# Kernel optimization log

Measured on AMD Instinct MI355X. Metric: run time of the kernel, lower is better.

## Reference

```python
import jax, jax.numpy as jnp
import numpy as np

N_NODES = 50000


def _gcn(x, row, col, w, b, n):
    # add self loops
    loops = jnp.arange(n, dtype=row.dtype)
    row = jnp.concatenate([row, loops])
    col = jnp.concatenate([col, loops])
    h = x @ w  # [N, out]
    deg = jax.ops.segment_sum(jnp.ones(col.shape, h.dtype), col, num_segments=n)
    dinv = jnp.where(deg > 0, deg ** -0.5, 0.0)
    norm = dinv[row] * dinv[col]  # [E+N]
    msg = norm[:, None] * h[row]
    out = jax.ops.segment_sum(msg, col, num_segments=n)
    return out + b


def _edgeconv(x, row, col, w1, b1, w2, b2, n):
    x_i = x[col]            # target features
    x_j = x[row]            # source features
    t = jnp.concatenate([x_i, x_j - x_i], axis=1)  # [E, 2*hidden]
    m = jax.nn.relu(t @ w1 + b1) @ w2 + b2          # [E, hidden]
    agg = jax.ops.segment_max(m, col, num_segments=n)
    # PyG fills empty segments with 0, segment_max fills with -inf
    return jnp.where(jnp.isfinite(agg), agg, 0.0)


def setup_inputs() -> dict:
    key = jax.random.key(0)
    ks = jax.random.split(key, 10)
    n, e = N_NODES, 800000
    cin, ch, cout = 32, 64, 16
    x = jax.random.normal(ks[0], (n, cin), dtype=jnp.float32)
    edge_index = jax.random.randint(ks[1], (2, e), 0, n, dtype=jnp.int64)

    def glorot(k, shape):
        lim = (6.0 / (shape[0] + shape[1])) ** 0.5
        return jax.random.uniform(k, shape, jnp.float32, -lim, lim)

    return {
        "x": x,
        "edge_index": edge_index,
        "gcn1_w": glorot(ks[2], (cin, ch)),
        "gcn1_b": jnp.zeros((ch,), jnp.float32),
        "edge_w1": glorot(ks[3], (2 * ch, ch)),
        "edge_b1": jnp.zeros((ch,), jnp.float32),
        "edge_w2": glorot(ks[4], (ch, ch)),
        "edge_b2": jnp.zeros((ch,), jnp.float32),
        "gcn2_w": glorot(ks[5], (ch, cout)),
        "gcn2_b": jnp.zeros((cout,), jnp.float32),
    }


def reference(x, edge_index, gcn1_w, gcn1_b, edge_w1, edge_b1, edge_w2, edge_b2, gcn2_w, gcn2_b):
    n = x.shape[0]
    row, col = edge_index[0], edge_index[1]
    h = jnp.tanh(_gcn(x, row, col, gcn1_w, gcn1_b, n))
    h = jax.nn.relu(_edgeconv(h, row, col, edge_w1, edge_b1, edge_w2, edge_b2, n))
    out = _gcn(h, row, col, gcn2_w, gcn2_b, n)
    return out
```

## Files before the change

kernel.cpp:

```cpp
#include <hip/hip_runtime.h>


typedef __attribute__((ext_vector_type(8))) short short8;
typedef __attribute__((ext_vector_type(4))) float f32x4;
typedef __attribute__((ext_vector_type(8))) _Float16 f16x8;
typedef __attribute__((ext_vector_type(4))) _Float16 f16x4;
typedef __attribute__((ext_vector_type(2))) _Float16 f16x2;

#define FILL_CH 4096

__device__ __forceinline__ unsigned short f2bf(float x) {
    unsigned int u = __float_as_uint(x);
    return (unsigned short)((u + 0x7FFFu + ((u >> 16) & 1u)) >> 16);
}
__device__ __forceinline__ float bf2f(unsigned short h) {
    return __uint_as_float(((unsigned int)h) << 16);
}
__device__ __forceinline__ void splitT(float u, short& hi, short& lo) {
    unsigned int ub = __float_as_uint(u);
    hi = (short)(ub >> 16);
    float r = u - __uint_as_float(ub & 0xFFFF0000u);
    lo = (short)(__float_as_uint(r) >> 16);
}
__device__ __forceinline__ f16x8 relu8(f16x8 v) {
    f16x8 z = {0, 0, 0, 0, 0, 0, 0, 0};
#if __has_builtin(__builtin_elementwise_max)
    return __builtin_elementwise_max(v, z);
#else
    f16x8 o;
#pragma unroll
    for (int j = 0; j < 8; ++j) o[j] = v[j] > (_Float16)0 ? v[j] : (_Float16)0;
    return o;
#endif
}

#define ROR_ADD(s, CTRL)                                                         \
    s += __int_as_float(__builtin_amdgcn_update_dpp(                             \
        0, __float_as_int(s), (CTRL), 0xf, 0xf, false))
#define ROR8_ADD(s) ROR_ADD(s, 0x128)

__global__ __launch_bounds__(256) void k_fill_a(
        const int* __restrict__ row, const int* __restrict__ col,
        const float4* __restrict__ x4, f16x4* __restrict__ xh4,
        int* __restrict__ bcnt, int* __restrict__ stage, int E, int m4, int nb) {
    __shared__ int cnt[512];
    __shared__ int base[512];
    int tid = threadIdx.x;
    int nth = gridDim.x * 256;
    for (int idx = blockIdx.x * 256 + tid; idx < m4; idx += nth) {
        float4 v = x4[idx];
        f16x4 o;
        o[0] = (_Float16)v.x; o[1] = (_Float16)v.y;
        o[2] = (_Float16)v.z; o[3] = (_Float16)v.w;
        xh4[idx] = o;
    }
    for (int i = tid; i < nb; i += 256) cnt[i] = 0;
    __syncthreads();
    int e0 = blockIdx.x * FILL_CH;
    int r[16], c[16];
#pragma unroll
    for (int i = 0; i < 16; ++i) {
        int e = e0 + tid + i * 256;
        if (e < E) {
            r[i] = row[e]; c[i] = col[e];
            atomicAdd(&cnt[c[i] >> 7], 1);
        } else c[i] = -1;
    }
    __syncthreads();
    for (int i = tid; i < nb; i += 256)
        base[i] = cnt[i] ? (i << 12) + atomicAdd(&bcnt[i], cnt[i]) : 0;
    __syncthreads();
#pragma unroll
    for (int i = 0; i < 16; ++i) {
        if (c[i] >= 0) {
            int b = c[i] >> 7;
            int lp = atomicAdd(&base[b], 1);
            stage[lp] = (r[i] << 7) | (c[i] & 127);
        }
    }
}

__global__ __launch_bounds__(256) void k_fill_b2(
        const int* __restrict__ bcnt, const int* __restrict__ stage,
        int* __restrict__ ptr, float* __restrict__ dinv, int* __restrict__ csr,
        int n, int nb, int E) {
    __shared__ int lcnt[128];
    __shared__ int lcur[128];
    __shared__ int wtotS;
    __shared__ int wsum[4];
    __shared__ int gbaseS;
    int b = blockIdx.x, tid = threadIdx.x;
    int lane = tid & 63, w = tid >> 6;
    int c0 = b << 7;
    int s0 = b << 12;
    int tot = bcnt[b];
    if (tid < 128) lcnt[tid] = 0;
    int acc = 0;
    if (tid < b && tid < nb) acc += bcnt[tid];
    int t2 = tid + 256;
    if (t2 < b && t2 < nb) acc += bcnt[t2];
#pragma unroll
    for (int off = 1; off < 64; off <<= 1) acc += __shfl_xor(acc, off);
    if (lane == 0) wsum[w] = acc;
    __syncthreads();
    if (tid == 0) {
        gbaseS = wsum[0] + wsum[1] + wsum[2] + wsum[3];
        if (b == nb - 1) ptr[n] = E;
    }
    for (int p = tid; p < tot; p += 256)
        atomicAdd(&lcnt[stage[s0 + p] & 127], 1);
    __syncthreads();
    int gbase = gbaseS;
    int v = (tid < 128) ? lcnt[tid] : 0;
    int s = v;
    for (int off = 1; off < 64; off <<= 1) {
        int t = __shfl_up(s, off, 64);
        if (lane >= off) s += t;
    }
    if (tid == 63) wtotS = s;
    __syncthreads();
    int excl = s - v + ((w == 1) ? wtotS : 0);
    if (tid < 128) {
        int c = c0 + tid;
        int basep = gbase + excl;
        lcur[tid] = basep;
        if (c < n) {
            ptr[c] = basep;
            dinv[c] = rsqrtf((float)(v + 1));
        }
    }
    __syncthreads();
    for (int p = tid; p < tot; p += 256) {
        int vv = stage[s0 + p];
        int pos = atomicAdd(&lcur[vv & 127], 1);
        csr[pos] = vv >> 7;
    }
}

__global__ __launch_bounds__(256) void k_gather32(
        const int* __restrict__ ptr, const int* __restrict__ csr_row,
        const float* __restrict__ x, const _Float16* __restrict__ xh,
        const float* __restrict__ dinv, float* __restrict__ agg, int n) {
    int lane = threadIdx.x & 63;
    int f4 = lane & 7, slot = lane >> 3;
    const f16x4* xh4 = (const f16x4*)xh;

    int nwaves = gridDim.x * 4;
    int wid = blockIdx.x * 4 + (threadIdx.x >> 6);
    if (wid >= n) return;

    int c = wid;
    int st = ptr[c], ed = ptr[c + 1];
    int r0 = (st + slot < ed) ? csr_row[st + slot] : 0;
    while (true) {
        int cn = c + nwaves;
        bool hasN = cn < n;
        int stn = 0, edn = 0;
        if (hasN) { stn = ptr[cn]; edn = ptr[cn + 1]; }

        float sx = 0.f, sy = 0.f, sz = 0.f, sw = 0.f;
        int p = st + slot;
        int r = r0;
        while (p < ed) {
            int rcur = r;
            int pn = p + 8;
            if (pn < ed) r = csr_row[pn];
            float dr = dinv[rcur];
            f16x4 xv = xh4[(size_t)rcur * 8 + f4];
            sx = fmaf(dr, (float)xv[0], sx);
            sy = fmaf(dr, (float)xv[1], sy);
            sz = fmaf(dr, (float)xv[2], sz);
            sw = fmaf(dr, (float)xv[3], sw);
            p = pn;
        }
        int r0n = 0;
        if (hasN && stn + slot < edn) r0n = csr_row[stn + slot];

        ROR8_ADD(sx); ROR8_ADD(sy); ROR8_ADD(sz); ROR8_ADD(sw);
#pragma unroll
        for (int off = 16; off < 64; off <<= 1) {
            sx += __shfl_xor(sx, off); sy += __shfl_xor(sy, off);
            sz += __shfl_xor(sz, off); sw += __shfl_xor(sw, off);
        }
        if (slot == 0) {
            float dv = dinv[c], d2 = dv * dv;
            float4 xv = ((const float4*)x)[(size_t)c * 8 + f4];
            float4 o;
            o.x = dv * sx + d2 * xv.x;
            o.y = dv * sy + d2 * xv.y;
            o.z = dv * sz + d2 * xv.z;
            o.w = dv * sw + d2 * xv.w;
            ((float4*)agg)[(size_t)c * 8 + f4] = o;
        }
        if (!hasN) break;
        c = cn; st = stn; ed = edn; r0 = r0n;
    }
}

__global__ __launch_bounds__(256, 1) void k_h1tab(
        const float* __restrict__ agg, const float* __restrict__ gw,
        const float* __restrict__ gb, const float* __restrict__ w1,
        const float* __restrict__ b1,
        _Float16* __restrict__ atab, _Float16* __restrict__ btab, int ntiles) {
    __shared__ float tileS[4][16 * 66];
    int lane = threadIdx.x & 63;
    int wv = threadIdx.x >> 6;
    int n16 = lane & 15, q = lane >> 4;
    float* T = tileS[wv];

    short8 gh[4], gl[4];
    float gbias[4];
#pragma unroll
    for (int t = 0; t < 4; ++t) {
        gbias[t] = gb[t * 16 + n16];
        short8 hh, ll;
#pragma unroll
        for (int j = 0; j < 8; ++j) {
            float w = gw[(q * 8 + j) * 64 + t * 16 + n16];
            unsigned short wh = f2bf(w);
            hh[j] = (short)wh;
            ll[j] = (short)f2bf(w - bf2f(wh));
        }
        gh[t] = hh; gl[t] = ll;
    }
    short8 th[4][2], tl[4][2], uh[4][2], ul[4][2];
    float bias1[4];
#pragma unroll
    for (int t = 0; t < 4; ++t) {
        bias1[t] = b1[t * 16 + n16];
#pragma unroll
        for (int ck = 0; ck < 2; ++ck) {
            short8 h1v, l1v, h2v, l2v;
#pragma unroll
            for (int j = 0; j < 8; ++j) {
                int d = ck * 32 + q * 8 + j;
                float wbv = w1[(64 + d) * 64 + t * 16 + n16];
                float wtv = w1[d * 64 + t * 16 + n16] - wbv;
                unsigned short x1 = f2bf(wtv);
                h1v[j] = (short)x1; l1v[j] = (short)f2bf(wtv - bf2f(x1));
                unsigned short x2 = f2bf(wbv);
                h2v[j] = (short)x2; l2v[j] = (short)f2bf(wbv - bf2f(x2));
            }
            th[t][ck] = h1v; tl[t][ck] = l1v;
            uh[t][ck] = h2v; ul[t][ck] = l2v;
        }
    }

    int nwaves = gridDim.x * 4;
    int wid = blockIdx.x * 4 + wv;
    for (int tile = wid; tile < ntiles; tile += nwaves) {
        int v0 = tile * 16;
        const float4* a4 = (const float4*)(agg + (size_t)(v0 + n16) * 32);
        float4 A0 = a4[2 * q], A1 = a4[2 * q + 1];
        float a[8] = {A0.x, A0.y, A0.z, A0.w, A1.x, A1.y, A1.z, A1.w};
        short8 ah, al;
#pragma unroll
        for (int j = 0; j < 8; ++j) { short h, l; splitT(a[j], h, l); ah[j] = h; al[j] = l; }
#pragma unroll
        for (int t = 0; t < 4; ++t) {
            f32x4 acc = (f32x4){gbias[t], gbias[t], gbias[t], gbias[t]};
            acc = __builtin_amdgcn_mfma_f32_16x16x32_bf16(ah, gh[t], acc, 0, 0, 0);
            acc = __builtin_amdgcn_mfma_f32_16x16x32_bf16(al, gh[t], acc, 0, 0, 0);
            acc = __builtin_amdgcn_mfma_f32_16x16x32_bf16(ah, gl[t], acc, 0, 0, 0);
#pragma unroll
            for (int i = 0; i < 4; ++i)
                T[(q * 4 + i) * 66 + t * 16 + n16] = tanhf(acc[i]);
        }
        float b[16];
#pragma unroll
        for (int j = 0; j < 8; ++j) {
            b[j]     = T[n16 * 66 + q * 8 + j];
            b[8 + j] = T[n16 * 66 + 32 + q * 8 + j];
        }
        short8 ah0, ah1, al0, al1;
#pragma unroll
        for (int j = 0; j < 8; ++j) {
            short h, l;
            splitT(b[j], h, l);      ah0[j] = h; al0[j] = l;
            splitT(b[8 + j], h, l);  ah1[j] = h; al1[j] = l;
        }
#pragma unroll
        for (int t = 0; t < 4; ++t) {
            f32x4 aa = (f32x4){bias1[t], bias1[t], bias1[t], bias1[t]};
            aa = __builtin_amdgcn_mfma_f32_16x16x32_bf16(ah0, th[t][0], aa, 0, 0, 0);
            aa = __builtin_amdgcn_mfma_f32_16x16x32_bf16(ah1, th[t][1], aa, 0, 0, 0);
            aa = __builtin_amdgcn_mfma_f32_16x16x32_bf16(al0, th[t][0], aa, 0, 0, 0);
            aa = __builtin_amdgcn_mfma_f32_16x16x32_bf16(al1, th[t][1], aa, 0, 0, 0);
            aa = __builtin_amdgcn_mfma_f32_16x16x32_bf16(ah0, tl[t][0], aa, 0, 0, 0);
            aa = __builtin_amdgcn_mfma_f32_16x16x32_bf16(ah1, tl[t][1], aa, 0, 0, 0);
            f32x4 bb = (f32x4){0.f, 0.f, 0.f, 0.f};
            bb = __builtin_amdgcn_mfma_f32_16x16x32_bf16(ah0, uh[t][0], bb, 0, 0, 0);
            bb = __builtin_amdgcn_mfma_f32_16x16x32_bf16(ah1, uh[t][1], bb, 0, 0, 0);
            bb = __builtin_amdgcn_mfma_f32_16x16x32_bf16(al0, uh[t][0], bb, 0, 0, 0);
            bb = __builtin_amdgcn_mfma_f32_16x16x32_bf16(al1, uh[t][1], bb, 0, 0, 0);
            bb = __builtin_amdgcn_mfma_f32_16x16x32_bf16(ah0, ul[t][0], bb, 0, 0, 0);
            bb = __builtin_amdgcn_mfma_f32_16x16x32_bf16(ah1, ul[t][1], bb, 0, 0, 0);
#pragma unroll
            for (int i = 0; i < 4; ++i) {
                size_t off = (size_t)(v0 + q * 4 + i) * 64 + t * 16 + n16;
                atab[off] = (_Float16)aa[i];
                btab[off] = (_Float16)bb[i];
            }
        }
    }
}

__global__ __launch_bounds__(256) void k_edge_mlp(
        const int* __restrict__ ptr, const int* __restrict__ csr_row,
        const _Float16* __restrict__ atab, const _Float16* __restrict__ btab,
        const float* __restrict__ w2, const float* __restrict__ b2,
        const float* __restrict__ wg, _Float16* __restrict__ h2h, int n) {
    int lane = threadIdx.x & 63;
    int n16 = lane & 15, q = lane >> 4;

    f16x8 wh[4][2];
    float bias[4];
    float wgf[4][4];
#pragma unroll
    for (int t = 0; t < 4; ++t) {
        bias[t] = b2[t * 16 + n16];
#pragma unroll
        for (int jj = 0; jj < 4; ++jj)
            wgf[t][jj] = wg[(t * 16 + n16) * 16 + q * 4 + jj];
#pragma unroll
        for (int ck = 0; ck < 2; ++ck) {
            f16x8 hh;
#pragma unroll
            for (int j = 0; j < 8; ++j)
                hh[j] = (_Float16)w2[(ck * 32 + q * 8 + j) * 64 + t * 16 + n16];
            wh[t][ck] = hh;
        }
    }
    const f32x4 z4 = (f32x4){0.f, 0.f, 0.f, 0.f};

    int nwaves = gridDim.x * 4;
    int wid = blockIdx.x * 4 + (threadIdx.x >> 6);
    if (wid >= n) return;

    int c = wid;
    int st = ptr[c], ed = ptr[c + 1];
    {
        int deg = ed - st;
        int nf = deg >> 4, rm = deg & 15;
        int rrem0 = (rm > 0 && n16 < rm) ? csr_row[st + (nf << 4) + n16] : 0;
        int r0 = (nf > 0) ? csr_row[st + n16] : 0;
        int r = r0, rrem = rrem0;
        while (true) {
            int cn = c + nwaves;
            bool hasN = cn < n;
            int stn = 0, edn = 0;
            if (hasN) { stn = ptr[cn]; edn = ptr[cn + 1]; }

            const f16x8* a8 = (const f16x8*)(atab + (size_t)c * 64);
            f16x8 A0 = a8[q], A1 = a8[4 + q];
            float red[4] = {0.f, 0.f, 0.f, 0.f};

            int deg2 = ed - st;
            int nfull = deg2 >> 4;
            int rem = deg2 & 15;
            for (int ft = 0; ft < nfull; ++ft) {
                int rcur = r;
                if (ft + 1 < nfull) r = csr_row[st + (ft + 1) * 16 + n16];
                const f16x8* b8 = (const f16x8*)(btab + (size_t)rcur * 64);
                f16x8 u0 = relu8(A0 + b8[q]);
                f16x8 u1 = relu8(A1 + b8[4 + q]);
                __builtin_amdgcn_s_setprio(1);
#pragma unroll
                for (int t = 0; t < 4; ++t) {
                    f32x4 a = __builtin_amdgcn_mfma_f32_16x16x32_f16(u0, wh[t][0], z4, 0, 0, 0);
                    a = __builtin_amdgcn_mfma_f32_16x16x32_f16(u1, wh[t][1], a, 0, 0, 0);
                    float mx = fmaxf(fmaxf(a[0], a[1]), fmaxf(a[2], a[3]));
                    red[t] = fmaxf(red[t], mx + bias[t]);
                }
                __builtin_amdgcn_s_setprio(0);
            }
            if (rem > 0) {
                f16x8 u0 = {0, 0, 0, 0, 0, 0, 0, 0};
                f16x8 u1 = {0, 0, 0, 0, 0, 0, 0, 0};
                if (n16 < rem) {
                    const f16x8* b8 = (const f16x8*)(btab + (size_t)rrem * 64);
                    u0 = relu8(A0 + b8[q]);
                    u1 = relu8(A1 + b8[4 + q]);
                }
                __builtin_amdgcn_s_setprio(1);
#pragma unroll
                for (int t = 0; t < 4; ++t) {
                    f32x4 a = __builtin_amdgcn_mfma_f32_16x16x32_f16(u0, wh[t][0], z4, 0, 0, 0);
                    a = __builtin_amdgcn_mfma_f32_16x16x32_f16(u1, wh[t][1], a, 0, 0, 0);
#pragma unroll
                    for (int i = 0; i < 4; ++i)
                        if (q * 4 + i < rem) red[t] = fmaxf(red[t], a[i] + bias[t]);
                }
                __builtin_amdgcn_s_setprio(0);
            }

            int rn = 0, rremn = 0;
            if (hasN) {
                int degn = edn - stn;
                int nfn = degn >> 4, rmn = degn & 15;
                if (rmn > 0 && n16 < rmn) rremn = csr_row[stn + (nfn << 4) + n16];
                if (nfn > 0) rn = csr_row[stn + n16];
            }

#pragma unroll
            for (int t = 0; t < 4; ++t) {
                red[t] = fmaxf(red[t], __shfl_xor(red[t], 16));
                red[t] = fmaxf(red[t], __shfl_xor(red[t], 32));
            }
            float part[4];
#pragma unroll
            for (int jj = 0; jj < 4; ++jj) {
                part[jj] = red[0] * wgf[0][jj];
                part[jj] = fmaf(red[1], wgf[1][jj], part[jj]);
                part[jj] = fmaf(red[2], wgf[2][jj], part[jj]);
                part[jj] = fmaf(red[3], wgf[3][jj], part[jj]);
                ROR_ADD(part[jj], 0x121);
                ROR_ADD(part[jj], 0x122);
                ROR_ADD(part[jj], 0x124);
                ROR_ADD(part[jj], 0x128);
            }
            if (n16 == 0) {
                f16x4 ph;
                ph[0] = (_Float16)part[0]; ph[1] = (_Float16)part[1];
                ph[2] = (_Float16)part[2]; ph[3] = (_Float16)part[3];
                ((f16x4*)(h2h + (size_t)c * 16))[q] = ph;
            }

            if (!hasN) break;
            c = cn; st = stn; ed = edn; r = rn; rrem = rremn;
        }
    }
}

__global__ __launch_bounds__(256) void k_gcn2_gather(
        const int* __restrict__ ptr, const int* __restrict__ csr_row,
        const _Float16* __restrict__ h2h, const float* __restrict__ dinv,
        const float* __restrict__ bg, float* __restrict__ out, int n) {
    int lane = threadIdx.x & 63;
    int f2 = lane & 7, slot = lane >> 3;
    const f16x2* h22 = (const f16x2*)h2h;

    int nwaves = gridDim.x * 4;
    int wid = blockIdx.x * 4 + (threadIdx.x >> 6);
    if (wid >= n) return;

    int c = wid;
    int st = ptr[c], ed = ptr[c + 1];
    int r0 = (st + slot < ed) ? csr_row[st + slot] : 0;
    while (true) {
        int cn = c + nwaves;
        bool hasN = cn < n;
        int stn = 0, edn = 0;
        if (hasN) { stn = ptr[cn]; edn = ptr[cn + 1]; }

        float sx = 0.f, sy = 0.f;
        int p = st + slot;
        int r = r0;
        while (p < ed) {
            int rcur = r;
            int pn = p + 8;
            if (pn < ed) r = csr_row[pn];
            float dr = dinv[rcur];
            f16x2 hv = h22[(size_t)rcur * 8 + f2];
            sx = fmaf(dr, (float)hv[0], sx);
            sy = fmaf(dr, (float)hv[1], sy);
            p = pn;
        }
        int r0n = 0;
        if (hasN && stn + slot < edn) r0n = csr_row[stn + slot];

        ROR8_ADD(sx); ROR8_ADD(sy);
#pragma unroll
        for (int off = 16; off < 64; off <<= 1) {
            sx += __shfl_xor(sx, off);
            sy += __shfl_xor(sy, off);
        }
        if (slot == 0) {
            float dv = dinv[c];
            f16x2 hv = h22[(size_t)c * 8 + f2];
            float2 o;
            o.x = bg[2 * f2]     + dv * (dv * (float)hv[0] + sx);
            o.y = bg[2 * f2 + 1] + dv * (dv * (float)hv[1] + sy);
            ((float2*)out)[(size_t)c * 8 + f2] = o;
        }
        if (!hasN) break;
        c = cn; st = stn; ed = edn; r0 = r0n;
    }
}

extern "C" void kernel_launch(void* const* d_in, const int* in_sizes, int n_in,
                              void* d_out, int out_size, void* d_ws, size_t ws_size,
                              hipStream_t stream) {
    const float* x   = (const float*)d_in[0];
    const int*   ei  = (const int*)d_in[1];
    const float* g1w = (const float*)d_in[2];
    const float* g1b = (const float*)d_in[3];
    const float* ew1 = (const float*)d_in[4];
    const float* eb1 = (const float*)d_in[5];
    const float* ew2 = (const float*)d_in[6];
    const float* eb2 = (const float*)d_in[7];
    const float* g2w = (const float*)d_in[8];
    const float* g2b = (const float*)d_in[9];
    float* out = (float*)d_out;
    float* ws  = (float*)d_ws;

    const int n = in_sizes[0] / 32;
    const int E = in_sizes[1] / 2;
    const int* row = ei;
    const int* col = ei + E;
    const int ntiles = (n + 15) / 16;
    const int nbuck = (n + 127) >> 7;

    size_t npad    = ((size_t)n + 63) & ~(size_t)63;
    size_t o_misc  = 0;
    size_t o_ptr   = 1024;
    size_t o_csr   = o_ptr + npad + 64;
    size_t o_dinv  = o_csr + (size_t)E;
    size_t o_atab  = o_dinv + npad;
    size_t o_btab  = o_atab + (size_t)n * 32;
    size_t o_agg   = o_btab + (size_t)n * 32;
    size_t o_xh    = o_agg + (size_t)n * 32;
    size_t o_h2h   = o_xh + (size_t)n * 16;
    size_t o_stage = o_h2h + (size_t)n * 8;

    int*      bcnt   = (int*)(ws + o_misc);
    int*      ptr    = (int*)(ws + o_ptr);
    int*      csr    = (int*)(ws + o_csr);
    float*    dinv   = ws + o_dinv;
    _Float16* atab   = (_Float16*)(ws + o_atab);
    _Float16* btab   = (_Float16*)(ws + o_btab);
    float*    agg    = ws + o_agg;
    _Float16* xh     = (_Float16*)(ws + o_xh);
    _Float16* h2h    = (_Float16*)(ws + o_h2h);
    int*      stage  = (int*)(ws + o_stage);

    int fill_nb = (E + FILL_CH - 1) / FILL_CH;
    int m4 = n * 8;

    hipMemsetAsync(bcnt, 0, 512 * sizeof(int), stream);
    k_fill_a<<<fill_nb, 256, 0, stream>>>(row, col, (const float4*)x, (f16x4*)xh,
                                          bcnt, stage, E, m4, nbuck);
    k_fill_b2<<<nbuck, 256, 0, stream>>>(bcnt, stage, ptr, dinv, csr, n, nbuck, E);
    k_gather32<<<2048, 256, 0, stream>>>(ptr, csr, x, xh, dinv, agg, n);
    k_h1tab<<<256, 256, 0, stream>>>(agg, g1w, g1b, ew1, eb1, atab, btab, ntiles);
    k_edge_mlp<<<2048, 256, 0, stream>>>(ptr, csr, atab, btab, ew2, eb2, g2w, h2h, n);
    k_gcn2_gather<<<2048, 256, 0, stream>>>(ptr, csr, h2h, dinv, g2b, out, n);
}
```

Before: 181.5 us.

## Pre-scale gathered node features by dinv so gathers skip per-edge dinv loads

The fp16 feature tables used by both GCN gathers are now pre-multiplied by the source node's dinv. The x conversion moves into k_fill_b2, where dinv is known, and h2h is scaled in the edge MLP epilogue. This removes a random dinv load and an FMA per edge in both gather loops, at the cost of moving the x conversion into a later kernel with fewer blocks. Rounding changes slightly because the scaled values are stored in fp16.

```diff
diff --git a/kernel.cpp b/kernel.cpp
--- a/kernel.cpp
+++ b/kernel.cpp
@@ -41,19 +41,10 @@
 
 __global__ __launch_bounds__(256) void k_fill_a(
         const int* __restrict__ row, const int* __restrict__ col,
-        const float4* __restrict__ x4, f16x4* __restrict__ xh4,
-        int* __restrict__ bcnt, int* __restrict__ stage, int E, int m4, int nb) {
+        int* __restrict__ bcnt, int* __restrict__ stage, int E, int nb) {
     __shared__ int cnt[512];
     __shared__ int base[512];
     int tid = threadIdx.x;
-    int nth = gridDim.x * 256;
-    for (int idx = blockIdx.x * 256 + tid; idx < m4; idx += nth) {
-        float4 v = x4[idx];
-        f16x4 o;
-        o[0] = (_Float16)v.x; o[1] = (_Float16)v.y;
-        o[2] = (_Float16)v.z; o[3] = (_Float16)v.w;
-        xh4[idx] = o;
-    }
     for (int i = tid; i < nb; i += 256) cnt[i] = 0;
     __syncthreads();
     int e0 = blockIdx.x * FILL_CH;
@@ -82,10 +73,12 @@
 
 __global__ __launch_bounds__(256) void k_fill_b2(
         const int* __restrict__ bcnt, const int* __restrict__ stage,
+        const float4* __restrict__ x4, f16x4* __restrict__ xh4,
         int* __restrict__ ptr, float* __restrict__ dinv, int* __restrict__ csr,
         int n, int nb, int E) {
     __shared__ int lcnt[128];
     __shared__ int lcur[128];
+    __shared__ float dinvS[128];
     __shared__ int wtotS;
     __shared__ int wsum[4];
     __shared__ int gbaseS;
@@ -124,9 +117,11 @@
         int c = c0 + tid;
         int basep = gbase + excl;
         lcur[tid] = basep;
+        float dv = rsqrtf((float)(v + 1));
+        dinvS[tid] = dv;
         if (c < n) {
             ptr[c] = basep;
-            dinv[c] = rsqrtf((float)(v + 1));
+            dinv[c] = dv;
         }
     }
     __syncthreads();
@@ -134,6 +129,16 @@
         int vv = stage[s0 + p];
         int pos = atomicAdd(&lcur[vv & 127], 1);
         csr[pos] = vv >> 7;
+    }
+    int cmax = n - c0; if (cmax > 128) cmax = 128;
+    for (int i = tid; i < cmax * 8; i += 256) {
+        int ci = i >> 3, j = i & 7;
+        float dv = dinvS[ci];
+        float4 xv = x4[(size_t)(c0 + ci) * 8 + j];
+        f16x4 o;
+        o[0] = (_Float16)(dv * xv.x); o[1] = (_Float16)(dv * xv.y);
+        o[2] = (_Float16)(dv * xv.z); o[3] = (_Float16)(dv * xv.w);
+        xh4[(size_t)(c0 + ci) * 8 + j] = o;
     }
 }
 
@@ -165,12 +170,11 @@
             int rcur = r;
             int pn = p + 8;
             if (pn < ed) r = csr_row[pn];
-            float dr = dinv[rcur];
             f16x4 xv = xh4[(size_t)rcur * 8 + f4];
-            sx = fmaf(dr, (float)xv[0], sx);
-            sy = fmaf(dr, (float)xv[1], sy);
-            sz = fmaf(dr, (float)xv[2], sz);
-            sw = fmaf(dr, (float)xv[3], sw);
+            sx += (float)xv[0];
+            sy += (float)xv[1];
+            sz += (float)xv[2];
+            sw += (float)xv[3];
             p = pn;
         }
         int r0n = 0;
@@ -309,7 +313,8 @@
         const int* __restrict__ ptr, const int* __restrict__ csr_row,
         const _Float16* __restrict__ atab, const _Float16* __restrict__ btab,
         const float* __restrict__ w2, const float* __restrict__ b2,
-        const float* __restrict__ wg, _Float16* __restrict__ h2h, int n) {
+        const float* __restrict__ wg, const float* __restrict__ dinv,
+        _Float16* __restrict__ h2h, int n) {
     int lane = threadIdx.x & 63;
     int n16 = lane & 15, q = lane >> 4;
 
@@ -339,6 +344,7 @@
 
     int c = wid;
     int st = ptr[c], ed = ptr[c + 1];
+    float dv = dinv[c];
     {
         int deg = ed - st;
         int nf = deg >> 4, rm = deg & 15;
@@ -349,7 +355,8 @@
             int cn = c + nwaves;
             bool hasN = cn < n;
             int stn = 0, edn = 0;
-            if (hasN) { stn = ptr[cn]; edn = ptr[cn + 1]; }
+            float dvn = 0.f;
+            if (hasN) { stn = ptr[cn]; edn = ptr[cn + 1]; dvn = dinv[cn]; }
 
             const f16x8* a8 = (const f16x8*)(atab + (size_t)c * 64);
             f16x8 A0 = a8[q], A1 = a8[4 + q];
@@ -421,13 +428,13 @@
             }
             if (n16 == 0) {
                 f16x4 ph;
-                ph[0] = (_Float16)part[0]; ph[1] = (_Float16)part[1];
-                ph[2] = (_Float16)part[2]; ph[3] = (_Float16)part[3];
+                ph[0] = (_Float16)(dv * part[0]); ph[1] = (_Float16)(dv * part[1]);
+                ph[2] = (_Float16)(dv * part[2]); ph[3] = (_Float16)(dv * part[3]);
                 ((f16x4*)(h2h + (size_t)c * 16))[q] = ph;
             }
 
             if (!hasN) break;
-            c = cn; st = stn; ed = edn; r = rn; rrem = rremn;
+            c = cn; st = stn; ed = edn; r = rn; rrem = rremn; dv = dvn;
         }
     }
 }
@@ -460,10 +467,9 @@
             int rcur = r;
             int pn = p + 8;
             if (pn < ed) r = csr_row[pn];
-            float dr = dinv[rcur];
             f16x2 hv = h22[(size_t)rcur * 8 + f2];
-            sx = fmaf(dr, (float)hv[0], sx);
-            sy = fmaf(dr, (float)hv[1], sy);
+            sx += (float)hv[0];
+            sy += (float)hv[1];
             p = pn;
         }
         int r0n = 0;
@@ -479,8 +485,8 @@
             float dv = dinv[c];
             f16x2 hv = h22[(size_t)c * 8 + f2];
             float2 o;
-            o.x = bg[2 * f2]     + dv * (dv * (float)hv[0] + sx);
-            o.y = bg[2 * f2 + 1] + dv * (dv * (float)hv[1] + sy);
+            o.x = bg[2 * f2]     + dv * ((float)hv[0] + sx);
+            o.y = bg[2 * f2 + 1] + dv * ((float)hv[1] + sy);
             ((float2*)out)[(size_t)c * 8 + f2] = o;
         }
         if (!hasN) break;
@@ -535,14 +541,14 @@
     int*      stage  = (int*)(ws + o_stage);
 
     int fill_nb = (E + FILL_CH - 1) / FILL_CH;
-    int m4 = n * 8;
 
     hipMemsetAsync(bcnt, 0, 512 * sizeof(int), stream);
-    k_fill_a<<<fill_nb, 256, 0, stream>>>(row, col, (const float4*)x, (f16x4*)xh,
-                                          bcnt, stage, E, m4, nbuck);
-    k_fill_b2<<<nbuck, 256, 0, stream>>>(bcnt, stage, ptr, dinv, csr, n, nbuck, E);
+    k_fill_a<<<fill_nb, 256, 0, stream>>>(row, col, bcnt, stage, E, nbuck);
+    k_fill_b2<<<nbuck, 256, 0, stream>>>(bcnt, stage, (const float4*)x, (f16x4*)xh,
+                                         ptr, dinv, csr, n, nbuck, E);
     k_gather32<<<2048, 256, 0, stream>>>(ptr, csr, x, xh, dinv, agg, n);
     k_h1tab<<<256, 256, 0, stream>>>(agg, g1w, g1b, ew1, eb1, atab, btab, ntiles);
-    k_edge_mlp<<<2048, 256, 0, stream>>>(ptr, csr, atab, btab, ew2, eb2, g2w, h2h, n);
+    k_edge_mlp<<<2048, 256, 0, stream>>>(ptr, csr, atab, btab, ew2, eb2, g2w,
+                                         dinv, h2h, n);
     k_gcn2_gather<<<2048, 256, 0, stream>>>(ptr, csr, h2h, dinv, g2b, out, n);
 }
```

New measurement: 179.6 us. Within noise of the previous version (-1.0%).
